# Performance work log

Measured on AMD Instinct MI355X. Metric: run time of the kernel, lower is better.

Reference implementation:

```python
import jax, jax.numpy as jnp
import numpy as np

B, T, D = 2, 2048, 2048
N, K, H = 16, 8, 128  # heads, kv heads, head_dim
F = 8192              # ffn hidden


def _apply_rope(x, positions, max_wavelength=10000):
    # x: [B, L, heads, H]; positions: [B, L]
    half = x.shape[-1] // 2
    freq_exponents = (2.0 / x.shape[-1]) * jnp.arange(half, dtype=jnp.float32)
    timescale = max_wavelength ** freq_exponents
    radians = positions.astype(jnp.float32)[..., None] / timescale[None, None, :]
    radians = radians[..., None, :]  # [B, L, 1, half]
    sin, cos = jnp.sin(radians), jnp.cos(radians)
    x1, x2 = jnp.split(x, 2, axis=-1)
    return jnp.concatenate([x1 * cos - x2 * sin, x2 * cos + x1 * sin], axis=-1)


def _rms_norm(x, scale):
    var = jnp.mean(jnp.square(x), axis=-1, keepdims=True)
    return x * jax.lax.rsqrt(var + 1e-6) * (1 + scale)


def setup_inputs() -> dict:
    key = jax.random.key(0)
    ks = jax.random.split(key, 8)
    s = 0.02
    x = jax.random.normal(ks[0], (B, T, D), jnp.float32)
    positions = jnp.broadcast_to(jnp.arange(T, dtype=jnp.int32)[None, :], (B, T))
    causal = jnp.tril(jnp.ones((T, T), dtype=bool))
    attn_mask = jnp.broadcast_to(causal[None, None, :, :], (B, 1, T, T))
    return {
        "x": x,
        "positions": positions,
        "attn_mask": attn_mask,
        "w_q": jax.random.normal(ks[1], (N, D, H), jnp.float32) * s,
        "w_kv": jax.random.normal(ks[2], (2, K, D, H), jnp.float32) * s,
        "w_attn_vec": jax.random.normal(ks[3], (N, H, D), jnp.float32) * s,
        "scale_pre_attn": jax.random.normal(ks[4], (D,), jnp.float32) * s,
        "scale_pre_ffw": jax.random.normal(ks[5], (D,), jnp.float32) * s,
        "w_gating": jax.random.normal(ks[6], (2, D, F), jnp.float32) * s,
        "w_linear": jax.random.normal(ks[7], (F, D), jnp.float32) * s,
    }


def reference(x, positions, attn_mask, w_q, w_kv, w_attn_vec,
              scale_pre_attn, scale_pre_ffw, w_gating, w_linear):
    # pre-attention RMSNorm
    xn = _rms_norm(x, scale_pre_attn)

    # GQA projections
    q = jnp.einsum('BTD,NDH->BTNH', xn, w_q)
    kv = jnp.einsum('BSD,eKDH->eBSKH', xn, w_kv)
    k, v = kv[0], kv[1]

    q = _apply_rope(q, positions) * (H ** -0.5)
    k = _apply_rope(k, positions)

    G = N // K
    q = q.reshape(q.shape[0], q.shape[1], K, G, H)  # B T K G H
    logits = jnp.einsum('BTKGH,BSKH->BKGTS', q, k).astype(jnp.float32)
    big_neg = -2.3819763e38
    masked = jnp.where(attn_mask[:, :, None, :, :], logits, big_neg)
    probs = jax.nn.softmax(masked, axis=-1).astype(k.dtype)
    enc = jnp.einsum('BKGTS,BSKH->BTKGH', probs, v)
    enc = enc.reshape(enc.shape[0], enc.shape[1], N, H)
    attn_out = jnp.einsum('BTNH,NHD->BTD', enc, w_attn_vec)

    # residual + pre-FFN RMSNorm + GeGLU FFN
    residual = x + attn_out
    h = _rms_norm(residual, scale_pre_ffw)
    gate = jax.nn.gelu(jnp.dot(h, w_gating[0]))
    act = gate * jnp.dot(h, w_gating[1])
    out = residual + jnp.dot(act, w_linear)
    return out
```

## Files before the change

### kernel.cpp

```cpp
#include <hip/hip_runtime.h>
#include <hip/hip_bf16.h>


typedef __attribute__((ext_vector_type(8))) short bf16x8;
typedef __attribute__((ext_vector_type(4))) float f32x4;

#define GLP(p) ((const __attribute__((address_space(1))) void*)(p))
#define LDSP(p) ((__attribute__((address_space(3))) void*)(p))
#define FBAR() do { asm volatile("" ::: "memory"); __builtin_amdgcn_s_barrier(); asm volatile("" ::: "memory"); } while (0)

__device__ __forceinline__ float bf2f(unsigned short h) {
  union { unsigned int u; float f; } v; v.u = ((unsigned int)h) << 16; return v.f;
}
__device__ __forceinline__ unsigned short f2bf(float f) {
  union { float f; unsigned int u; } v; v.f = f;
  unsigned int r = v.u + 0x7fffu + ((v.u >> 16) & 1u);
  return (unsigned short)(r >> 16);
}
__device__ __forceinline__ float gelu_f(float x) {
  float t = tanhf(0.7978845608028654f * (x + 0.044715f * x * x * x));
  return 0.5f * x * (1.f + t);
}

template <int IN_F32>
__global__ __launch_bounds__(256) void rmsnorm_kernel(const void* __restrict__ x_,
                                                      const float* __restrict__ scale,
                                                      unsigned short* __restrict__ out) {
  int row = blockIdx.x, tid = threadIdx.x;
  float f[8]; float ss = 0.f;
  if (IN_F32) {
    const float* xr = (const float*)x_ + (size_t)row * 2048 + tid * 8;
#pragma unroll
    for (int i = 0; i < 8; ++i) { f[i] = xr[i]; ss += f[i] * f[i]; }
  } else {
    const unsigned short* xr = (const unsigned short*)x_ + (size_t)row * 2048;
    bf16x8 xv = *(const bf16x8*)(xr + tid * 8);
#pragma unroll
    for (int i = 0; i < 8; ++i) { f[i] = bf2f((unsigned short)xv[i]); ss += f[i] * f[i]; }
  }
#pragma unroll
  for (int off = 32; off >= 1; off >>= 1) ss += __shfl_xor(ss, off);
  __shared__ float red[4];
  if ((tid & 63) == 0) red[tid >> 6] = ss;
  __syncthreads();
  ss = red[0] + red[1] + red[2] + red[3];
  float r = rsqrtf(ss * (1.f / 2048.f) + 1e-6f);
  const float* sv = scale + tid * 8;
  bf16x8 o;
#pragma unroll
  for (int i = 0; i < 8; ++i) o[i] = (short)f2bf(f[i] * r * (1.f + sv[i]));
  *(bf16x8*)(out + (size_t)row * 2048 + tid * 8) = o;
}

__global__ __launch_bounds__(256) void transpose_cast_kernel(const float* __restrict__ in,
                                                             unsigned short* __restrict__ out,
                                                             int R, int ldi, long ibs, long obs) {
  __shared__ float tile[32][33];
  int z = blockIdx.z;
  const float* ip = in + (size_t)z * ibs;
  unsigned short* op = out + (size_t)z * obs;
  int c0 = blockIdx.x * 32, r0 = blockIdx.y * 32;
  int tx = threadIdx.x, ty = threadIdx.y;
#pragma unroll
  for (int i = 0; i < 32; i += 8)
    tile[ty + i][tx] = ip[(size_t)(r0 + ty + i) * ldi + (c0 + tx)];
  __syncthreads();
#pragma unroll
  for (int i = 0; i < 32; i += 8)
    op[(size_t)(c0 + ty + i) * R + (r0 + tx)] = f2bf(tile[tx][ty + i]);
}

__global__ __launch_bounds__(256) void vtrans_kernel(const unsigned short* __restrict__ qkv,
                                                     unsigned short* __restrict__ vT) {
  __shared__ unsigned short tile[32][33];
  int z = blockIdx.z, bb = z >> 3, kh = z & 7;
  int s0 = blockIdx.x * 32, h0 = blockIdx.y * 32;
  int tx = threadIdx.x, ty = threadIdx.y;
  const unsigned short* ip = qkv + ((size_t)bb * 2048) * 4096 + 3072 + kh * 128;
  unsigned short* op = vT + (size_t)z * 128 * 2048;
#pragma unroll
  for (int i = 0; i < 32; i += 8)
    tile[ty + i][tx] = ip[(size_t)(s0 + ty + i) * 4096 + h0 + tx];
  __syncthreads();
#pragma unroll
  for (int i = 0; i < 32; i += 8)
    op[(size_t)(h0 + ty + i) * 2048 + s0 + tx] = tile[tx][ty + i];
}

template <int BM, int MODE, int OUT_F32, int ADD_F32>
__global__ __launch_bounds__(512, 2) void gemm8p(const unsigned short* __restrict__ A,
                                                 const unsigned short* __restrict__ BT,
                                                 int Kd, int ldc, int gx,
                                                 void* __restrict__ out_,
                                                 const void* __restrict__ add_) {
  constexpr int MR = BM / 32;
  constexpr int MH = MR / 2;
  constexpr int ASZ = BM * 64;
  constexpr int BSZ = 256 * 64;
  __shared__ unsigned short lds[2 * ASZ + 2 * BSZ];
  unsigned short* aBuf0 = lds;
  unsigned short* aBuf1 = lds + ASZ;
  unsigned short* bBuf0 = lds + 2 * ASZ;
  unsigned short* bBuf1 = lds + 2 * ASZ + BSZ;

  int tid = threadIdx.x;
  int lane = tid & 63, w = tid >> 6;
  int quad = lane >> 4, l16 = lane & 15;
  int wm = w >> 2, wn = w & 3;
  int l8 = lane >> 3;

  int nwg = gridDim.x;
  int id = blockIdx.x;
  int swzid = (id & 7) * (nwg >> 3) + (id >> 3);
  int bx = swzid % gx, by = swzid / gx;
  long rowBase = (long)by * BM, colBase = (long)bx * 256;

  int csw = ((lane & 7) ^ l8) * 8;
  int rwB = (w >> 2) * 64 + (w & 3) * 8 + l8;
  int rwA = (BM == 256) ? (w * 8 + l8) : rwB;
  const unsigned short* aSrc = A + (rowBase + rwA) * (size_t)Kd + csw;
  const unsigned short* bSrc = BT + (colBase + rwB) * (size_t)Kd + csw;

  auto stgA = [&](unsigned short* dst, int h, int tt) {
    if (BM == 256) {
      __builtin_amdgcn_global_load_lds(GLP(aSrc + (size_t)(h * 64) * Kd + (size_t)tt * 64),
                                       LDSP(dst + (h * 128 + w * 8) * 64), 16, 0, 0);
      __builtin_amdgcn_global_load_lds(GLP(aSrc + (size_t)(128 + h * 64) * Kd + (size_t)tt * 64),
                                       LDSP(dst + (h * 128 + 64 + w * 8) * 64), 16, 0, 0);
    } else {
      __builtin_amdgcn_global_load_lds(GLP(aSrc + (size_t)(h * 32) * Kd + (size_t)tt * 64),
                                       LDSP(dst + (h * 64 + w * 8) * 64), 16, 0, 0);
    }
  };
  auto stgB = [&](unsigned short* dst, int h, int tt) {
    __builtin_amdgcn_global_load_lds(GLP(bSrc + (size_t)(h * 32) * Kd + (size_t)tt * 64),
                                     LDSP(dst + (h * 128 + w * 8) * 64), 16, 0, 0);
    __builtin_amdgcn_global_load_lds(GLP(bSrc + (size_t)(128 + h * 32) * Kd + (size_t)tt * 64),
                                     LDSP(dst + (h * 128 + 64 + w * 8) * 64), 16, 0, 0);
  };

  int swq0 = (quad * 8) ^ ((l16 & 7) * 8);
  int swq1 = (32 + quad * 8) ^ ((l16 & 7) * 8);
  auto rdA = [&](const unsigned short* cur, int i, int kk) -> bf16x8 {
    int rho = (BM == 256) ? ((i >> 2) * 128 + wm * 64 + (i & 3) * 16 + l16)
                          : ((i >> 1) * 64 + wm * 32 + (i & 1) * 16 + l16);
    return *(const bf16x8*)(cur + rho * 64 + (kk ? swq1 : swq0));
  };
  auto rdB = [&](const unsigned short* cur, int j, int kk) -> bf16x8 {
    int rho = (j >> 1) * 128 + wn * 32 + (j & 1) * 16 + l16;
    return *(const bf16x8*)(cur + rho * 64 + (kk ? swq1 : swq0));
  };

  f32x4 acc[MR][4];
#pragma unroll
  for (int i = 0; i < MR; ++i)
#pragma unroll
    for (int j = 0; j < 4; ++j) acc[i][j] = (f32x4){0.f, 0.f, 0.f, 0.f};

  stgA(aBuf0, 0, 0); stgB(bBuf0, 0, 0); stgB(bBuf0, 1, 0); stgA(aBuf0, 1, 0);
  stgA(aBuf1, 0, 1); stgB(bBuf1, 0, 1);
  if constexpr (BM == 256) asm volatile("s_waitcnt vmcnt(4)" ::: "memory");
  else                     asm volatile("s_waitcnt vmcnt(3)" ::: "memory");
  FBAR();

  int NT = Kd >> 6;
  bf16x8 af[MH][2], bfr0[2][2], bfr1[2][2];
  for (int t = 0; t < NT; ++t) {
    unsigned short* aCur = (t & 1) ? aBuf1 : aBuf0;
    unsigned short* bCur = (t & 1) ? bBuf1 : bBuf0;
    unsigned short* aNxt = (t & 1) ? aBuf0 : aBuf1;
    unsigned short* bNxt = (t & 1) ? bBuf0 : bBuf1;

#pragma unroll
    for (int i = 0; i < MH; ++i) { af[i][0] = rdA(aCur, i, 0); af[i][1] = rdA(aCur, i, 1); }
#pragma unroll
    for (int j = 0; j < 2; ++j) { bfr0[j][0] = rdB(bCur, j, 0); bfr0[j][1] = rdB(bCur, j, 1); }
    if (t + 1 < NT) stgB(bNxt, 1, t + 1);
    FBAR();
    __builtin_amdgcn_s_setprio(1);
#pragma unroll
    for (int kk = 0; kk < 2; ++kk)
#pragma unroll
      for (int i = 0; i < MH; ++i)
#pragma unroll
        for (int j = 0; j < 2; ++j)
          acc[i][j] = __builtin_amdgcn_mfma_f32_16x16x32_bf16(af[i][kk], bfr0[j][kk], acc[i][j], 0, 0, 0);
    __builtin_amdgcn_s_setprio(0);

#pragma unroll
    for (int j = 0; j < 2; ++j) { bfr1[j][0] = rdB(bCur, j + 2, 0); bfr1[j][1] = rdB(bCur, j + 2, 1); }
    if (t + 1 < NT) stgA(aNxt, 1, t + 1);
    FBAR();
    __builtin_amdgcn_s_setprio(1);
#pragma unroll
    for (int kk = 0; kk < 2; ++kk)
#pragma unroll
      for (int i = 0; i < MH; ++i)
#pragma unroll
        for (int j = 0; j < 2; ++j)
          acc[i][j + 2] = __builtin_amdgcn_mfma_f32_16x16x32_bf16(af[i][kk], bfr1[j][kk], acc[i][j + 2], 0, 0, 0);
    __builtin_amdgcn_s_setprio(0);

#pragma unroll
    for (int i = 0; i < MH; ++i) { af[i][0] = rdA(aCur, MH + i, 0); af[i][1] = rdA(aCur, MH + i, 1); }
    if (t + 2 < NT) stgA(aCur, 0, t + 2);
    FBAR();
    __builtin_amdgcn_s_setprio(1);
#pragma unroll
    for (int kk = 0; kk < 2; ++kk)
#pragma unroll
      for (int i = 0; i < MH; ++i)
#pragma unroll
        for (int j = 0; j < 2; ++j)
          acc[MH + i][j] = __builtin_amdgcn_mfma_f32_16x16x32_bf16(af[i][kk], bfr0[j][kk], acc[MH + i][j], 0, 0, 0);
    __builtin_amdgcn_s_setprio(0);

    if (t + 2 < NT) {
      stgB(bCur, 0, t + 2);
      if constexpr (BM == 256) asm volatile("s_waitcnt vmcnt(4)" ::: "memory");
      else                     asm volatile("s_waitcnt vmcnt(3)" ::: "memory");
    } else {
      asm volatile("s_waitcnt vmcnt(0)" ::: "memory");
    }
    FBAR();
    __builtin_amdgcn_s_setprio(1);
#pragma unroll
    for (int kk = 0; kk < 2; ++kk)
#pragma unroll
      for (int i = 0; i < MH; ++i)
#pragma unroll
        for (int j = 0; j < 2; ++j)
          acc[MH + i][j + 2] = __builtin_amdgcn_mfma_f32_16x16x32_bf16(af[i][kk], bfr1[j][kk], acc[MH + i][j + 2], 0, 0, 0);
    __builtin_amdgcn_s_setprio(0);
  }

  float* outf = (float*)out_;
  unsigned short* outb = (unsigned short*)out_;
  const float* addf = (const float*)add_;
  const unsigned short* addb = (const unsigned short*)add_;
  long orow = rowBase + wm * (BM / 2);
  long ocol = colBase + wn * 64 + l16;
#pragma unroll
  for (int i = 0; i < MR; ++i)
#pragma unroll
    for (int j = 0; j < 4; ++j)
#pragma unroll
      for (int rr = 0; rr < 4; ++rr) {
        long row = orow + i * 16 + quad * 4 + rr;
        long col = ocol + j * 16;
        long idx = row * (long)ldc + col;
        float v = acc[i][j][rr];
        if (MODE == 0) {
          outb[idx] = f2bf(v);
        } else if (MODE == 1) {
          v += (ADD_F32 ? addf[idx] : bf2f(addb[idx]));
          if (OUT_F32) outf[idx] = v; else outb[idx] = f2bf(v);
        } else {
          outb[idx] = f2bf(gelu_f(v) * bf2f(outb[idx]));
        }
      }
}

__global__ __launch_bounds__(256) void rope_kernel(unsigned short* __restrict__ qkv,
                                                   const int* __restrict__ pos) {
  int gid = blockIdx.x * 256 + threadIdx.x;
  int hp = gid & 63;
  int rh = gid >> 6;
  int row = rh / 24;
  int head = rh - row * 24;
  float p = (float)pos[row];
  long cb; float sc;
  if (head < 16) { cb = (long)head * 128; sc = 0.08838834764831845f; }
  else { cb = 2048 + (long)(head - 16) * 128; sc = 1.f; }
  unsigned short* ptr = qkv + (long)row * 4096 + cb;
  float inv = exp2f(-(float)hp * (13.287712379549449f / 64.f));
  float ang = p * inv;
  float s = sinf(ang), c = cosf(ang);
  float x1 = bf2f(ptr[hp]), x2 = bf2f(ptr[hp + 64]);
  ptr[hp]      = f2bf((x1 * c - x2 * s) * sc);
  ptr[hp + 64] = f2bf((x2 * c + x1 * s) * sc);
}

__global__ __launch_bounds__(256, 3) void attn_kernel(const unsigned short* __restrict__ qkv,
                                                      const unsigned short* __restrict__ vT,
                                                      unsigned short* __restrict__ enc) {
  extern __shared__ char smem[];
  unsigned short* sK = (unsigned short*)smem;
  unsigned short* sVT = sK + 64 * 128;
  unsigned short* sP = sVT + 64 * 128;

  int qt = (int)gridDim.x - 1 - blockIdx.x, n = blockIdx.y, b = blockIdx.z;
  int tid = threadIdx.x, lane = tid & 63, w = tid >> 6;
  int quad = lane >> 4, l16 = lane & 15;
  int kh = n >> 1;
  long rowQ = (long)b * 2048 + (long)qt * 64;

  bf16x8 qf[4];
  {
    const unsigned short* qp = qkv + (rowQ + w * 16 + l16) * 4096 + n * 128 + quad * 8;
#pragma unroll
    for (int ks = 0; ks < 4; ++ks) qf[ks] = *(const bf16x8*)(qp + ks * 32);
  }
  f32x4 oacc[8];
#pragma unroll
  for (int t = 0; t < 8; ++t) oacc[t] = (f32x4){0.f, 0.f, 0.f, 0.f};
  float m_r[4], l_r[4];
#pragma unroll
  for (int r = 0; r < 4; ++r) { m_r[r] = -1e30f; l_r[r] = 0.f; }

  for (int st = 0; st <= qt; ++st) {
    __syncthreads();
#pragma unroll
    for (int it = 0; it < 4; ++it) {
      int idx = it * 256 + tid;
      int r = idx >> 4, c = idx & 15;
      bf16x8 kv8 = *(const bf16x8*)(qkv + ((long)b * 2048 + st * 64 + r) * 4096 + 2048 + kh * 128 + c * 8);
      *(bf16x8*)(sK + r * 128 + ((c ^ (r & 7)) * 8)) = kv8;
    }
#pragma unroll
    for (int it = 0; it < 4; ++it) {
      int idx = it * 256 + tid;
      int h = idx >> 3, c = idx & 7;
      bf16x8 vv8 = *(const bf16x8*)(vT + ((long)(b * 8 + kh) * 128 + h) * 2048 + st * 64 + c * 8);
      *(bf16x8*)(sVT + h * 64 + ((c ^ (h & 7)) * 8)) = vv8;
    }
    __syncthreads();

    f32x4 sacc[4];
#pragma unroll
    for (int nt = 0; nt < 4; ++nt) sacc[nt] = (f32x4){0.f, 0.f, 0.f, 0.f};
#pragma unroll
    for (int ks = 0; ks < 4; ++ks)
#pragma unroll
      for (int nt = 0; nt < 4; ++nt) {
        int r = nt * 16 + l16;
        bf16x8 kf = *(const bf16x8*)(sK + r * 128 + (((ks * 4 + quad) ^ (r & 7)) * 8));
        sacc[nt] = __builtin_amdgcn_mfma_f32_16x16x32_bf16(qf[ks], kf, sacc[nt], 0, 0, 0);
      }

    float p[4][4];
#pragma unroll
    for (int r = 0; r < 4; ++r) {
      int qrow = w * 16 + quad * 4 + r;
      float mx = -1e30f;
#pragma unroll
      for (int nt = 0; nt < 4; ++nt) {
        float v = sacc[nt][r];
        if (st * 64 + nt * 16 + l16 > qt * 64 + qrow) v = -1e30f;
        p[nt][r] = v;
        mx = fmaxf(mx, v);
      }
      mx = fmaxf(mx, __shfl_xor(mx, 1));
      mx = fmaxf(mx, __shfl_xor(mx, 2));
      mx = fmaxf(mx, __shfl_xor(mx, 4));
      mx = fmaxf(mx, __shfl_xor(mx, 8));
      float m_new = fmaxf(m_r[r], mx);
      float al = __expf(m_r[r] - m_new);
      float sum = 0.f;
#pragma unroll
      for (int nt = 0; nt < 4; ++nt) { p[nt][r] = __expf(p[nt][r] - m_new); sum += p[nt][r]; }
      sum += __shfl_xor(sum, 1);
      sum += __shfl_xor(sum, 2);
      sum += __shfl_xor(sum, 4);
      sum += __shfl_xor(sum, 8);
      l_r[r] = al * l_r[r] + sum;
      m_r[r] = m_new;
#pragma unroll
      for (int nt = 0; nt < 8; ++nt) oacc[nt][r] *= al;
    }

#pragma unroll
    for (int nt = 0; nt < 4; ++nt)
#pragma unroll
      for (int r = 0; r < 4; ++r)
        sP[(w * 16 + quad * 4 + r) * 68 + nt * 16 + l16] = f2bf(p[nt][r]);

#pragma unroll
    for (int ks = 0; ks < 2; ++ks) {
      bf16x8 pf = *(const bf16x8*)(sP + (w * 16 + l16) * 68 + ks * 32 + quad * 8);
#pragma unroll
      for (int nt = 0; nt < 8; ++nt) {
        int hh = nt * 16 + l16;
        bf16x8 vf = *(const bf16x8*)(sVT + hh * 64 + (((ks * 4 + quad) ^ (hh & 7)) * 8));
        oacc[nt] = __builtin_amdgcn_mfma_f32_16x16x32_bf16(pf, vf, oacc[nt], 0, 0, 0);
      }
    }
  }

#pragma unroll
  for (int r = 0; r < 4; ++r) {
    float invl = 1.f / l_r[r];
    long trow = rowQ + w * 16 + quad * 4 + r;
#pragma unroll
    for (int nt = 0; nt < 8; ++nt)
      enc[trow * 2048 + n * 128 + nt * 16 + l16] = f2bf(oacc[nt][r] * invl);
  }
}

extern "C" void kernel_launch(void* const* d_in, const int* in_sizes, int n_in,
                              void* d_out, int out_size, void* d_ws, size_t ws_size,
                              hipStream_t stream) {
  const float* x = (const float*)d_in[0];
  const int* positions = (const int*)d_in[1];
  const float* wq = (const float*)d_in[3];
  const float* wkv = (const float*)d_in[4];
  const float* wav = (const float*)d_in[5];
  const float* s_attn = (const float*)d_in[6];
  const float* s_ffw = (const float*)d_in[7];
  const float* wg = (const float*)d_in[8];
  const float* wl = (const float*)d_in[9];
  float* outp = (float*)d_out;

  char* ws = (char*)d_ws;
  size_t o = 0;
  unsigned short* XN = (unsigned short*)(ws + o);    o += (size_t)4096 * 2048 * 2;
  unsigned short* WQKVT = (unsigned short*)(ws + o); o += (size_t)4096 * 2048 * 2;
  unsigned short* WAVT = (unsigned short*)(ws + o);  o += (size_t)2048 * 2048 * 2;
  unsigned short* WGT = (unsigned short*)(ws + o);   o += (size_t)8192 * 2048 * 2;
  unsigned short* QKV = (unsigned short*)(ws + o);   o += (size_t)4096 * 4096 * 2;
  unsigned short* VTb = (unsigned short*)(ws + o);   o += (size_t)16 * 128 * 2048 * 2;
  unsigned short* ACT = (unsigned short*)(ws + o);   o += (size_t)4096 * 8192 * 2;
  unsigned short* ENC = WQKVT;
  unsigned short* RES = QKV;
  unsigned short* HB = XN;

  dim3 b256(256), bT(32, 8);

  rmsnorm_kernel<1><<<4096, b256, 0, stream>>>(x, s_attn, XN);

  transpose_cast_kernel<<<dim3(4, 64, 16), bT, 0, stream>>>(wq, WQKVT, 2048, 128, 262144L, 262144L);
  transpose_cast_kernel<<<dim3(4, 64, 8), bT, 0, stream>>>(wkv, WQKVT + (size_t)2048 * 2048, 2048, 128, 262144L, 262144L);
  transpose_cast_kernel<<<dim3(4, 64, 8), bT, 0, stream>>>(wkv + (size_t)8 * 262144, WQKVT + (size_t)3072 * 2048, 2048, 128, 262144L, 262144L);
  transpose_cast_kernel<<<dim3(64, 64, 1), bT, 0, stream>>>(wav, WAVT, 2048, 2048, 0L, 0L);

  gemm8p<256, 0, 0, 0><<<256, 512, 0, stream>>>(XN, WQKVT, 2048, 4096, 16, QKV, nullptr);

  vtrans_kernel<<<dim3(64, 4, 16), bT, 0, stream>>>(QKV, VTb);

  rope_kernel<<<24576, b256, 0, stream>>>(QKV, positions);

  attn_kernel<<<dim3(32, 16, 2), b256, 41472, stream>>>(QKV, VTb, ENC);

  gemm8p<128, 1, 0, 1><<<256, 512, 0, stream>>>(ENC, WAVT, 2048, 2048, 8, RES, x);

  rmsnorm_kernel<0><<<4096, b256, 0, stream>>>(RES, s_ffw, HB);

  for (int half = 0; half < 2; ++half) {
    long f0 = (long)half * 4096;
    transpose_cast_kernel<<<dim3(128, 64, 1), bT, 0, stream>>>(wg + f0, WGT, 2048, 8192, 0L, 0L);
    transpose_cast_kernel<<<dim3(128, 64, 1), bT, 0, stream>>>(wg + (size_t)2048 * 8192 + f0,
                                                               WGT + (size_t)4096 * 2048, 2048, 8192, 0L, 0L);
    gemm8p<256, 0, 0, 0><<<256, 512, 0, stream>>>(HB, WGT + (size_t)4096 * 2048, 2048, 8192, 16, ACT + f0, nullptr);
    gemm8p<256, 2, 0, 0><<<256, 512, 0, stream>>>(HB, WGT, 2048, 8192, 16, ACT + f0, nullptr);
  }

  transpose_cast_kernel<<<dim3(64, 256, 1), bT, 0, stream>>>(wl, WGT, 8192, 2048, 0L, 0L);
  gemm8p<128, 1, 1, 0><<<256, 512, 0, stream>>>(ACT, WGT, 8192, 2048, 8, outp, RES);
}
```

Measured before the change: 1.064 ms.

## Enlarge attention query tile to 128 rows and prefetch K/V through registers

The attention kernel now gives each block 128 query rows instead of 64, so each wave handles two 16-row groups and every K/V tile loaded into shared memory serves twice as many queries. The next K/V tile is also loaded into registers while the current one is computed, then written to shared memory between barriers, so global load latency overlaps with the MFMA work. In exchange, register pressure rises (launch bounds drop from 3 to 2 blocks per CU), the grid is halved to 512 blocks, and the causal diagonal tile wastes more masked work per block.

```diff
diff --git a/kernel.cpp b/kernel.cpp
--- a/kernel.cpp
+++ b/kernel.cpp
@@ -281,120 +281,163 @@
   ptr[hp + 64] = f2bf((x2 * c + x1 * s) * sc);
 }
 
-__global__ __launch_bounds__(256, 3) void attn_kernel(const unsigned short* __restrict__ qkv,
+__global__ __launch_bounds__(256, 2) void attn_kernel(const unsigned short* __restrict__ qkv,
                                                       const unsigned short* __restrict__ vT,
                                                       unsigned short* __restrict__ enc) {
   extern __shared__ char smem[];
   unsigned short* sK = (unsigned short*)smem;
   unsigned short* sVT = sK + 64 * 128;
-  unsigned short* sP = sVT + 64 * 128;
+  unsigned short* sP = sVT + 128 * 64;
 
   int qt = (int)gridDim.x - 1 - blockIdx.x, n = blockIdx.y, b = blockIdx.z;
   int tid = threadIdx.x, lane = tid & 63, w = tid >> 6;
   int quad = lane >> 4, l16 = lane & 15;
   int kh = n >> 1;
-  long rowQ = (long)b * 2048 + (long)qt * 64;
-
-  bf16x8 qf[4];
-  {
-    const unsigned short* qp = qkv + (rowQ + w * 16 + l16) * 4096 + n * 128 + quad * 8;
-#pragma unroll
-    for (int ks = 0; ks < 4; ++ks) qf[ks] = *(const bf16x8*)(qp + ks * 32);
+  long rowQ = (long)b * 2048 + (long)qt * 128;
+
+  bf16x8 qf[2][4];
+#pragma unroll
+  for (int g = 0; g < 2; ++g) {
+    const unsigned short* qp = qkv + (rowQ + w * 32 + g * 16 + l16) * 4096 + n * 128 + quad * 8;
+#pragma unroll
+    for (int ks = 0; ks < 4; ++ks) qf[g][ks] = *(const bf16x8*)(qp + ks * 32);
   }
-  f32x4 oacc[8];
-#pragma unroll
-  for (int t = 0; t < 8; ++t) oacc[t] = (f32x4){0.f, 0.f, 0.f, 0.f};
-  float m_r[4], l_r[4];
-#pragma unroll
-  for (int r = 0; r < 4; ++r) { m_r[r] = -1e30f; l_r[r] = 0.f; }
-
-  for (int st = 0; st <= qt; ++st) {
-    __syncthreads();
-#pragma unroll
-    for (int it = 0; it < 4; ++it) {
-      int idx = it * 256 + tid;
-      int r = idx >> 4, c = idx & 15;
-      bf16x8 kv8 = *(const bf16x8*)(qkv + ((long)b * 2048 + st * 64 + r) * 4096 + 2048 + kh * 128 + c * 8);
-      *(bf16x8*)(sK + r * 128 + ((c ^ (r & 7)) * 8)) = kv8;
-    }
-#pragma unroll
-    for (int it = 0; it < 4; ++it) {
-      int idx = it * 256 + tid;
-      int h = idx >> 3, c = idx & 7;
-      bf16x8 vv8 = *(const bf16x8*)(vT + ((long)(b * 8 + kh) * 128 + h) * 2048 + st * 64 + c * 8);
-      *(bf16x8*)(sVT + h * 64 + ((c ^ (h & 7)) * 8)) = vv8;
-    }
-    __syncthreads();
-
-    f32x4 sacc[4];
-#pragma unroll
-    for (int nt = 0; nt < 4; ++nt) sacc[nt] = (f32x4){0.f, 0.f, 0.f, 0.f};
+  f32x4 oacc[2][8];
+#pragma unroll
+  for (int g = 0; g < 2; ++g)
+#pragma unroll
+    for (int t = 0; t < 8; ++t) oacc[g][t] = (f32x4){0.f, 0.f, 0.f, 0.f};
+  float m_r[2][4], l_r[2][4];
+#pragma unroll
+  for (int g = 0; g < 2; ++g)
+#pragma unroll
+    for (int r = 0; r < 4; ++r) { m_r[g][r] = -1e30f; l_r[g][r] = 0.f; }
+
+  int rK[4], cK[4], hV[4], cV[4];
+#pragma unroll
+  for (int it = 0; it < 4; ++it) {
+    int idx = it * 256 + tid;
+    rK[it] = idx >> 4; cK[it] = idx & 15;
+    hV[it] = idx >> 3; cV[it] = idx & 7;
+  }
+  const unsigned short* kbase = qkv + ((long)b * 2048) * 4096 + 2048 + kh * 128;
+  const unsigned short* vbase = vT + ((long)(b * 8 + kh) * 128) * 2048;
+
+  bf16x8 kreg[4], vreg[4];
+  auto loadKV = [&](int st) {
+#pragma unroll
+    for (int it = 0; it < 4; ++it)
+      kreg[it] = *(const bf16x8*)(kbase + ((long)(st * 64 + rK[it])) * 4096 + cK[it] * 8);
+#pragma unroll
+    for (int it = 0; it < 4; ++it)
+      vreg[it] = *(const bf16x8*)(vbase + (long)hV[it] * 2048 + st * 64 + cV[it] * 8);
+  };
+  auto storeKV = [&]() {
+#pragma unroll
+    for (int it = 0; it < 4; ++it)
+      *(bf16x8*)(sK + rK[it] * 128 + ((cK[it] ^ (rK[it] & 7)) * 8)) = kreg[it];
+#pragma unroll
+    for (int it = 0; it < 4; ++it)
+      *(bf16x8*)(sVT + hV[it] * 64 + ((cV[it] ^ (hV[it] & 7)) * 8)) = vreg[it];
+  };
+
+  int nst = 2 * qt + 2;
+  loadKV(0);
+  storeKV();
+  __syncthreads();
+
+  for (int st = 0; st < nst; ++st) {
+    if (st + 1 < nst) loadKV(st + 1);
+
+    f32x4 sacc[2][4];
+#pragma unroll
+    for (int g = 0; g < 2; ++g)
+#pragma unroll
+      for (int nt = 0; nt < 4; ++nt) sacc[g][nt] = (f32x4){0.f, 0.f, 0.f, 0.f};
 #pragma unroll
     for (int ks = 0; ks < 4; ++ks)
 #pragma unroll
       for (int nt = 0; nt < 4; ++nt) {
         int r = nt * 16 + l16;
         bf16x8 kf = *(const bf16x8*)(sK + r * 128 + (((ks * 4 + quad) ^ (r & 7)) * 8));
-        sacc[nt] = __builtin_amdgcn_mfma_f32_16x16x32_bf16(qf[ks], kf, sacc[nt], 0, 0, 0);
+        sacc[0][nt] = __builtin_amdgcn_mfma_f32_16x16x32_bf16(qf[0][ks], kf, sacc[0][nt], 0, 0, 0);
+        sacc[1][nt] = __builtin_amdgcn_mfma_f32_16x16x32_bf16(qf[1][ks], kf, sacc[1][nt], 0, 0, 0);
       }
 
-    float p[4][4];
-#pragma unroll
-    for (int r = 0; r < 4; ++r) {
-      int qrow = w * 16 + quad * 4 + r;
-      float mx = -1e30f;
-#pragma unroll
-      for (int nt = 0; nt < 4; ++nt) {
-        float v = sacc[nt][r];
-        if (st * 64 + nt * 16 + l16 > qt * 64 + qrow) v = -1e30f;
-        p[nt][r] = v;
-        mx = fmaxf(mx, v);
+#pragma unroll
+    for (int g = 0; g < 2; ++g)
+#pragma unroll
+      for (int r = 0; r < 4; ++r) {
+        int qrow = w * 32 + g * 16 + quad * 4 + r;
+        float mx = -1e30f;
+#pragma unroll
+        for (int nt = 0; nt < 4; ++nt) {
+          float v = sacc[g][nt][r];
+          if (st * 64 + nt * 16 + l16 > qt * 128 + qrow) v = -1e30f;
+          sacc[g][nt][r] = v;
+          mx = fmaxf(mx, v);
+        }
+        mx = fmaxf(mx, __shfl_xor(mx, 1));
+        mx = fmaxf(mx, __shfl_xor(mx, 2));
+        mx = fmaxf(mx, __shfl_xor(mx, 4));
+        mx = fmaxf(mx, __shfl_xor(mx, 8));
+        float m_new = fmaxf(m_r[g][r], mx);
+        float al = __expf(m_r[g][r] - m_new);
+        float sum = 0.f;
+#pragma unroll
+        for (int nt = 0; nt < 4; ++nt) {
+          float e = __expf(sacc[g][nt][r] - m_new);
+          sacc[g][nt][r] = e;
+          sum += e;
+        }
+        sum += __shfl_xor(sum, 1);
+        sum += __shfl_xor(sum, 2);
+        sum += __shfl_xor(sum, 4);
+        sum += __shfl_xor(sum, 8);
+        l_r[g][r] = al * l_r[g][r] + sum;
+        m_r[g][r] = m_new;
+#pragma unroll
+        for (int nt = 0; nt < 8; ++nt) oacc[g][nt][r] *= al;
       }
-      mx = fmaxf(mx, __shfl_xor(mx, 1));
-      mx = fmaxf(mx, __shfl_xor(mx, 2));
-      mx = fmaxf(mx, __shfl_xor(mx, 4));
-      mx = fmaxf(mx, __shfl_xor(mx, 8));
-      float m_new = fmaxf(m_r[r], mx);
-      float al = __expf(m_r[r] - m_new);
-      float sum = 0.f;
-#pragma unroll
-      for (int nt = 0; nt < 4; ++nt) { p[nt][r] = __expf(p[nt][r] - m_new); sum += p[nt][r]; }
-      sum += __shfl_xor(sum, 1);
-      sum += __shfl_xor(sum, 2);
-      sum += __shfl_xor(sum, 4);
-      sum += __shfl_xor(sum, 8);
-      l_r[r] = al * l_r[r] + sum;
-      m_r[r] = m_new;
-#pragma unroll
-      for (int nt = 0; nt < 8; ++nt) oacc[nt][r] *= al;
-    }
-
-#pragma unroll
-    for (int nt = 0; nt < 4; ++nt)
-#pragma unroll
-      for (int r = 0; r < 4; ++r)
-        sP[(w * 16 + quad * 4 + r) * 68 + nt * 16 + l16] = f2bf(p[nt][r]);
+
+#pragma unroll
+    for (int g = 0; g < 2; ++g)
+#pragma unroll
+      for (int nt = 0; nt < 4; ++nt)
+#pragma unroll
+        for (int r = 0; r < 4; ++r)
+          sP[(w * 32 + g * 16 + quad * 4 + r) * 68 + nt * 16 + l16] = f2bf(sacc[g][nt][r]);
 
 #pragma unroll
     for (int ks = 0; ks < 2; ++ks) {
-      bf16x8 pf = *(const bf16x8*)(sP + (w * 16 + l16) * 68 + ks * 32 + quad * 8);
+      bf16x8 pf0 = *(const bf16x8*)(sP + (w * 32 + l16) * 68 + ks * 32 + quad * 8);
+      bf16x8 pf1 = *(const bf16x8*)(sP + (w * 32 + 16 + l16) * 68 + ks * 32 + quad * 8);
 #pragma unroll
       for (int nt = 0; nt < 8; ++nt) {
         int hh = nt * 16 + l16;
         bf16x8 vf = *(const bf16x8*)(sVT + hh * 64 + (((ks * 4 + quad) ^ (hh & 7)) * 8));
-        oacc[nt] = __builtin_amdgcn_mfma_f32_16x16x32_bf16(pf, vf, oacc[nt], 0, 0, 0);
+        oacc[0][nt] = __builtin_amdgcn_mfma_f32_16x16x32_bf16(pf0, vf, oacc[0][nt], 0, 0, 0);
+        oacc[1][nt] = __builtin_amdgcn_mfma_f32_16x16x32_bf16(pf1, vf, oacc[1][nt], 0, 0, 0);
       }
     }
+
+    if (st + 1 < nst) {
+      __syncthreads();
+      storeKV();
+      __syncthreads();
+    }
   }
 
 #pragma unroll
-  for (int r = 0; r < 4; ++r) {
-    float invl = 1.f / l_r[r];
-    long trow = rowQ + w * 16 + quad * 4 + r;
-#pragma unroll
-    for (int nt = 0; nt < 8; ++nt)
-      enc[trow * 2048 + n * 128 + nt * 16 + l16] = f2bf(oacc[nt][r] * invl);
-  }
+  for (int g = 0; g < 2; ++g)
+#pragma unroll
+    for (int r = 0; r < 4; ++r) {
+      float invl = 1.f / l_r[g][r];
+      long trow = rowQ + w * 32 + g * 16 + quad * 4 + r;
+#pragma unroll
+      for (int nt = 0; nt < 8; ++nt)
+        enc[trow * 2048 + n * 128 + nt * 16 + l16] = f2bf(oacc[g][nt][r] * invl);
+    }
 }
 
 extern "C" void kernel_launch(void* const* d_in, const int* in_sizes, int n_in,
@@ -439,7 +482,7 @@
 
   rope_kernel<<<24576, b256, 0, stream>>>(QKV, positions);
 
-  attn_kernel<<<dim3(32, 16, 2), b256, 41472, stream>>>(QKV, VTb, ENC);
+  attn_kernel<<<dim3(16, 16, 2), b256, 50176, stream>>>(QKV, VTb, ENC);
 
   gemm8p<128, 1, 0, 1><<<256, 512, 0, stream>>>(ENC, WAVT, 2048, 2048, 8, RES, x);
 
```

Measured after the change: 1.181 ms. 11.0% more time.
